# Performance work log

Hardware: AMD Instinct MI355X
Metric: run time of the kernel (lower is better)

Reference implementation:

```python
import jax, jax.numpy as jnp
import numpy as np
import math

IN_DIM = 256
HID_DIM = 256
NUM_EDGE_TYPES = 3
HEADS = 8
HEAD_DIM = HID_DIM // HEADS  # 32
QK_DIM = (NUM_EDGE_TYPES + 1) * HID_DIM  # 1024
N = 4096


def _glorot(key, shape):
    # torch_geometric-style glorot: uniform(-a, a), a = sqrt(6/(fan_in+fan_out)) over last two dims
    a = math.sqrt(6.0 / (shape[-2] + shape[-1]))
    return jax.random.uniform(key, shape, jnp.float32, -a, a)


def setup_inputs() -> dict:
    key = jax.random.key(0)
    ks = jax.random.split(key, 8)
    return {
        "input_x": jax.random.normal(ks[0], (N, IN_DIM), jnp.float32),
        "pe_Q": jax.random.normal(ks[1], (N, NUM_EDGE_TYPES * HID_DIM), jnp.float32),
        "pe_K": jax.random.normal(ks[2], (N, NUM_EDGE_TYPES * HID_DIM), jnp.float32),
        "A": jnp.zeros((N, N), jnp.int32),  # accepted by forward but unused
        "WQ": _glorot(ks[3], (HEADS, QK_DIM, HEAD_DIM)),
        "WK": _glorot(ks[4], (HEADS, QK_DIM, HEAD_DIM)),
        "WV": _glorot(ks[5], (HEADS, IN_DIM, HEAD_DIM)),
        "Q_bias": jnp.zeros((HEADS, 1, HEAD_DIM), jnp.float32),
        "K_bias": jnp.zeros((HEADS, 1, HEAD_DIM), jnp.float32),
        "V_bias": jnp.zeros((HEADS, 1, HEAD_DIM), jnp.float32),
        "lin_w": _glorot(ks[6], (HID_DIM, HID_DIM)),
        "lin_b": jnp.zeros((HID_DIM,), jnp.float32),
    }


def reference(input_x, pe_Q, pe_K, A, WQ, WK, WV, Q_bias, K_bias, V_bias, lin_w, lin_b):
    x_Q = jnp.concatenate([input_x, pe_Q], axis=-1)  # [N, QK_DIM]
    x_K = jnp.concatenate([input_x, pe_K], axis=-1)  # [N, QK_DIM]
    Q = jnp.einsum('nd,hdk->hnk', x_Q, WQ) + Q_bias   # [H, N, hd]
    K = jnp.einsum('nd,hdk->hnk', x_K, WK) + K_bias   # [H, N, hd]
    V = jnp.einsum('nd,hdk->hnk', input_x, WV) + V_bias
    scores = jnp.einsum('hnk,hmk->hnm', Q, K) / math.sqrt(HID_DIM)  # [H, N, N]
    scores = scores - jax.lax.stop_gradient(jnp.max(scores, axis=-1, keepdims=True))
    attn = jax.nn.softmax(scores, axis=-1)
    attn = jnp.where(jnp.isnan(attn), jnp.zeros_like(attn), attn)
    attn_x = jnp.einsum('hnm,hmk->hnk', attn, V)      # [H, N, hd]
    # cat(list over heads, dim=1) -> [N, H*hd] with head-major column order
    x_cat = jnp.transpose(attn_x, (1, 0, 2)).reshape(attn_x.shape[1], -1)
    return x_cat @ lin_w.T + lin_b
```

## Files before the change

### kernel.cpp

```cpp
#include <hip/hip_runtime.h>
#include <hip/hip_bf16.h>

typedef __attribute__((ext_vector_type(8))) short bf16x8;
typedef __attribute__((ext_vector_type(4))) float f32x4;

__device__ __forceinline__ unsigned short f2b(float f) {
    union { float f; unsigned int u; } v; v.f = f;
    unsigned int u = v.u;
    unsigned int r = (u + 0x7FFFu + ((u >> 16) & 1u)) >> 16;
    return (unsigned short)r;
}
__device__ __forceinline__ float b2f(unsigned short h) {
    union { unsigned int u; float f; } v; v.u = ((unsigned int)h) << 16;
    return v.f;
}
__device__ __forceinline__ unsigned pk2(float a, float b) {
    union { __hip_bfloat162 h; unsigned u; } c;
    c.h = __float22bfloat162_rn(make_float2(a, b));
    return c.u;
}

__global__ __launch_bounds__(256) void prep_main(
    const float* __restrict__ WQ, const float* __restrict__ WK,
    const float* __restrict__ WV, const float* __restrict__ LW,
    const float* __restrict__ Qb, const float* __restrict__ Kb,
    const float* __restrict__ Vb,
    const float* __restrict__ x, const float* __restrict__ peQ,
    const float* __restrict__ peK,
    unsigned short* __restrict__ WQt, unsigned short* __restrict__ WKt,
    unsigned short* __restrict__ WVt, unsigned short* __restrict__ LWt,
    unsigned short* __restrict__ Bq, unsigned short* __restrict__ Bk,
    unsigned short* __restrict__ Bv,
    unsigned short* __restrict__ xb, unsigned short* __restrict__ peQb,
    unsigned short* __restrict__ peKb) {
    int b = blockIdx.x, t = threadIdx.x;
    if (b < 288) {
        const float* W; unsigned short* Wt; int h, d0, D; float sc = 1.0f;
        if (b < 128)      { W = WQ; Wt = WQt; h = b >> 4;   d0 = (b & 15) * 64; D = 1024; sc = 0.0625f; }
        else if (b < 256) { int bb = b - 128; W = WK; Wt = WKt; h = bb >> 4; d0 = (bb & 15) * 64; D = 1024; }
        else              { int bb = b - 256; W = WV; Wt = WVt; h = bb >> 2; d0 = (bb & 3) * 64;  D = 256; }
        __shared__ float Ts[32][65];
        int dr = t >> 2, k0 = (t & 3) * 8;
        const float* src = W + (h * D + d0 + dr) * 32 + k0;
        float4 u0 = *(const float4*)src;
        float4 u1 = *(const float4*)(src + 4);
        Ts[k0 + 0][dr] = u0.x; Ts[k0 + 1][dr] = u0.y; Ts[k0 + 2][dr] = u0.z; Ts[k0 + 3][dr] = u0.w;
        Ts[k0 + 4][dr] = u1.x; Ts[k0 + 5][dr] = u1.y; Ts[k0 + 6][dr] = u1.z; Ts[k0 + 7][dr] = u1.w;
        __syncthreads();
        int k = t >> 3, dc = (t & 7) * 8;
        union { unsigned short s[8]; uint4 v; } pk;
#pragma unroll
        for (int i = 0; i < 8; i++) pk.s[i] = f2b(Ts[k][dc + i] * sc);
        *(uint4*)(Wt + (h * 32 + k) * D + d0 + dc) = pk.v;
    } else if (b < 320) {
        int base = (b - 288) * 2048 + t * 8;
        const float* sp = LW + base;
        float4 u0 = *(const float4*)sp;
        float4 u1 = *(const float4*)(sp + 4);
        union { unsigned u[4]; uint4 v; } pk;
        pk.u[0] = pk2(u0.x, u0.y); pk.u[1] = pk2(u0.z, u0.w);
        pk.u[2] = pk2(u1.x, u1.y); pk.u[3] = pk2(u1.z, u1.w);
        *(uint4*)(LWt + base) = pk.v;
    } else if (b == 320) {
        Bq[t] = f2b(Qb[t] * 0.0625f); Bk[t] = f2b(Kb[t]); Bv[t] = f2b(Vb[t]);
    } else {
        int idx = (b - 321) * 2048 + t * 8;
        const float* sp; unsigned short* dp;
        if (idx < 1048576)      { sp = x + idx;                dp = xb + idx; }
        else if (idx < 4194304) { sp = peQ + (idx - 1048576);  dp = peQb + (idx - 1048576); }
        else                    { sp = peK + (idx - 4194304);  dp = peKb + (idx - 4194304); }
        float4 u0 = *(const float4*)sp;
        float4 u1 = *(const float4*)(sp + 4);
        union { unsigned u[4]; uint4 v; } pk;
        pk.u[0] = pk2(u0.x, u0.y); pk.u[1] = pk2(u0.z, u0.w);
        pk.u[2] = pk2(u1.x, u1.y); pk.u[3] = pk2(u1.z, u1.w);
        *(uint4*)dp = pk.v;
    }
}

__global__ __launch_bounds__(256) void prep_fb(
    const float* __restrict__ WQ, const float* __restrict__ WK,
    const float* __restrict__ WV,
    const float* __restrict__ Qb, const float* __restrict__ Kb,
    const float* __restrict__ Vb,
    unsigned short* __restrict__ WQt, unsigned short* __restrict__ WKt,
    unsigned short* __restrict__ WVt,
    unsigned short* __restrict__ Bq, unsigned short* __restrict__ Bk,
    unsigned short* __restrict__ Bv) {
    int b = blockIdx.x, t = threadIdx.x;
    if (b < 288) {
        const float* W; unsigned short* Wt; int h, d0, D; float sc = 1.0f;
        if (b < 128)      { W = WQ; Wt = WQt; h = b >> 4;   d0 = (b & 15) * 64; D = 1024; sc = 0.0625f; }
        else if (b < 256) { int bb = b - 128; W = WK; Wt = WKt; h = bb >> 4; d0 = (bb & 15) * 64; D = 1024; }
        else              { int bb = b - 256; W = WV; Wt = WVt; h = bb >> 2; d0 = (bb & 3) * 64;  D = 256; }
        __shared__ float Ts[32][65];
        int dr = t >> 2, k0 = (t & 3) * 8;
        const float* src = W + (h * D + d0 + dr) * 32 + k0;
        float4 u0 = *(const float4*)src;
        float4 u1 = *(const float4*)(src + 4);
        Ts[k0 + 0][dr] = u0.x; Ts[k0 + 1][dr] = u0.y; Ts[k0 + 2][dr] = u0.z; Ts[k0 + 3][dr] = u0.w;
        Ts[k0 + 4][dr] = u1.x; Ts[k0 + 5][dr] = u1.y; Ts[k0 + 6][dr] = u1.z; Ts[k0 + 7][dr] = u1.w;
        __syncthreads();
        int k = t >> 3, dc = (t & 7) * 8;
        union { unsigned short s[8]; uint4 v; } pk;
#pragma unroll
        for (int i = 0; i < 8; i++) pk.s[i] = f2b(Ts[k][dc + i] * sc);
        *(uint4*)(Wt + (h * 32 + k) * D + d0 + dc) = pk.v;
    } else {
        Bq[t] = f2b(Qb[t] * 0.0625f); Bk[t] = f2b(Kb[t]); Bv[t] = f2b(Vb[t]);
    }
}

template <bool ABF16>
__global__ __launch_bounds__(256) void proj_fused(
    const void* __restrict__ xv,
    const void* __restrict__ peQv, const void* __restrict__ peKv,
    const unsigned short* __restrict__ WQt, const unsigned short* __restrict__ WKt,
    const unsigned short* __restrict__ WVt,
    const unsigned short* __restrict__ Bq, const unsigned short* __restrict__ Bk,
    const unsigned short* __restrict__ Bv,
    unsigned short* __restrict__ Qc, unsigned short* __restrict__ KV) {
    __shared__ unsigned short As[64 * 72];
    __shared__ unsigned short Bs[64 * 72];
    int bx = blockIdx.x;
    int which = bx >> 8, bb = bx & 255;
    const void* A1; const unsigned short* Bt; const unsigned short* bias; int K;
    if (which == 0)      { A1 = peQv; Bt = WQt; bias = Bq; K = 1024; }
    else if (which == 1) { A1 = peKv; Bt = WKt; bias = Bk; K = 1024; }
    else                 { A1 = peQv; Bt = WVt; bias = Bv; K = 256; }
    int mb = bb & 63, nb = bb >> 6;
    int m0 = mb * 64, n0 = nb * 64;
    int t = threadIdx.x, w = t >> 6, lane = t & 63;
    int ln = lane & 15, q8 = (lane >> 4) * 8;
    int wm = (w >> 1) * 32, wn = (w & 1) * 32;
    int sr = t >> 3, sc = (t & 7) * 8;
    f32x4 acc[2][2];
#pragma unroll
    for (int i = 0; i < 2; i++)
#pragma unroll
        for (int j = 0; j < 2; j++) acc[i][j] = (f32x4){0.f, 0.f, 0.f, 0.f};
    for (int kb = 0; kb < K; kb += 64) {
#pragma unroll
        for (int half = 0; half < 2; half++) {
            int r = sr + half * 32;
            int c = kb + sc;
            if (ABF16) {
                const unsigned short* ap = (c < 256)
                    ? ((const unsigned short*)xv + (m0 + r) * 256 + c)
                    : ((const unsigned short*)A1 + (m0 + r) * 768 + (c - 256));
                *(uint4*)&As[r * 72 + sc] = *(const uint4*)ap;
            } else {
                const float* ap = (c < 256)
                    ? ((const float*)xv + (m0 + r) * 256 + c)
                    : ((const float*)A1 + (m0 + r) * 768 + (c - 256));
                float4 u0 = *(const float4*)ap;
                float4 u1 = *(const float4*)(ap + 4);
                union { unsigned u[4]; uint4 v; } pk;
                pk.u[0] = pk2(u0.x, u0.y); pk.u[1] = pk2(u0.z, u0.w);
                pk.u[2] = pk2(u1.x, u1.y); pk.u[3] = pk2(u1.z, u1.w);
                *(uint4*)&As[r * 72 + sc] = pk.v;
            }
            *(uint4*)&Bs[r * 72 + sc] = *(const uint4*)(Bt + (n0 + r) * K + c);
        }
        __syncthreads();
#pragma unroll
        for (int ks = 0; ks < 64; ks += 32) {
            bf16x8 a[2], b[2];
#pragma unroll
            for (int i = 0; i < 2; i++) {
                a[i] = *(const bf16x8*)&As[(wm + i * 16 + ln) * 72 + ks + q8];
                b[i] = *(const bf16x8*)&Bs[(wn + i * 16 + ln) * 72 + ks + q8];
            }
#pragma unroll
            for (int i = 0; i < 2; i++)
#pragma unroll
                for (int j = 0; j < 2; j++)
                    acc[i][j] = __builtin_amdgcn_mfma_f32_16x16x32_bf16(a[i], b[j], acc[i][j], 0, 0, 0);
        }
        __syncthreads();
    }
#pragma unroll
    for (int j = 0; j < 2; j++) {
        int ncol = n0 + wn + j * 16 + ln;
        float bv = b2f(bias[ncol]);
        int h2 = ncol >> 5, din = ncol & 31;
#pragma unroll
        for (int i = 0; i < 2; i++) {
            int rbase = m0 + wm + i * 16 + ((lane >> 4) * 4);
            if (which == 0) {
#pragma unroll
                for (int r = 0; r < 4; r++)
                    Qc[(rbase + r) * 256 + ncol] = f2b(acc[i][j][r] + bv);
            } else if (which == 1) {
#pragma unroll
                for (int r = 0; r < 4; r++) {
                    int key = rbase + r;
                    int T2 = key >> 6, k6 = key & 63;
                    int kt = ((k6 >> 2) & 1) + ((k6 >> 4) & 2);
                    int ln2 = ((k6 >> 3) & 3) * 4 + (k6 & 3);
                    int addr = (h2 * 64 + T2) * 4096 + kt * 512
                             + ((din >> 3) * 16 + ln2) * 8 + (din & 7);
                    KV[addr] = f2b(acc[i][j][r] + bv);
                }
            } else {
                int key = rbase;
                int T2 = key >> 6, k6 = key & 63;
                int chunk = 4 + ((din >> 4) << 1) + ((k6 >> 5) & 1);
                int lane2 = ((k6 >> 3) & 3) * 16 + (din & 15);
                int addr = (h2 * 64 + T2) * 4096 + chunk * 512 + lane2 * 8 + (k6 & 7);
                uint2 vv;
                vv.x = pk2(acc[i][j][0] + bv, acc[i][j][1] + bv);
                vv.y = pk2(acc[i][j][2] + bv, acc[i][j][3] + bv);
                *(uint2*)(KV + addr) = vv;
            }
        }
    }
}

__global__ __launch_bounds__(256, 4) void attn_kernel(
    const unsigned short* __restrict__ Qc,
    const unsigned short* __restrict__ KV,
    unsigned short* __restrict__ Xc) {
    __shared__ float Om[4][32][33];
    __shared__ float Ls[4][32];
    int head = blockIdx.x >> 7;
    int qb = blockIdx.x & 127;
    int t = threadIdx.x, w = t >> 6, lane = t & 63;
    int ln = lane & 15, quad = lane >> 4, q8 = quad * 8;
    int q0 = qb * 32;
    bf16x8 qfv[2];
#pragma unroll
    for (int qf = 0; qf < 2; qf++)
        qfv[qf] = *(const bf16x8*)(Qc + (q0 + qf * 16 + ln) * 256 + head * 32 + q8);
    const unsigned short* kv = KV + (head * 64 + w * 16) * 4096 + lane * 8;
    f32x4 o[2][2];
#pragma unroll
    for (int qf = 0; qf < 2; qf++)
#pragma unroll
        for (int hh = 0; hh < 2; hh++) o[qf][hh] = (f32x4){0.f, 0.f, 0.f, 0.f};
    const f32x4 z = {0.f, 0.f, 0.f, 0.f};
    f32x4 lacc[2]; lacc[0] = z; lacc[1] = z;
    bf16x8 k0 = *(const bf16x8*)(kv + 0);
    bf16x8 k1 = *(const bf16x8*)(kv + 512);
    bf16x8 k2 = *(const bf16x8*)(kv + 1024);
    bf16x8 k3 = *(const bf16x8*)(kv + 1536);
    bf16x8 v0 = *(const bf16x8*)(kv + 2048);
    bf16x8 v1 = *(const bf16x8*)(kv + 2560);
    bf16x8 v2 = *(const bf16x8*)(kv + 3072);
    bf16x8 v3 = *(const bf16x8*)(kv + 3584);
#pragma unroll 1
    for (int it = 0; it < 16; it++) {
        int nit = (it < 15) ? (it + 1) : 15;
        const unsigned short* nkv = kv + nit * 4096;
        bf16x8 nk0 = *(const bf16x8*)(nkv + 0);
        bf16x8 nk1 = *(const bf16x8*)(nkv + 512);
        bf16x8 nk2 = *(const bf16x8*)(nkv + 1024);
        bf16x8 nk3 = *(const bf16x8*)(nkv + 1536);
        bf16x8 nv0 = *(const bf16x8*)(nkv + 2048);
        bf16x8 nv1 = *(const bf16x8*)(nkv + 2560);
        bf16x8 nv2 = *(const bf16x8*)(nkv + 3072);
        bf16x8 nv3 = *(const bf16x8*)(nkv + 3584);
#pragma unroll
        for (int qf = 0; qf < 2; qf++) {
            f32x4 s0 = __builtin_amdgcn_mfma_f32_16x16x32_bf16(k0, qfv[qf], z, 0, 0, 0);
            f32x4 s1 = __builtin_amdgcn_mfma_f32_16x16x32_bf16(k1, qfv[qf], z, 0, 0, 0);
            f32x4 s2 = __builtin_amdgcn_mfma_f32_16x16x32_bf16(k2, qfv[qf], z, 0, 0, 0);
            f32x4 s3 = __builtin_amdgcn_mfma_f32_16x16x32_bf16(k3, qfv[qf], z, 0, 0, 0);
            float p0[4], p1[4], p2[4], p3[4];
#pragma unroll
            for (int r = 0; r < 4; r++) {
                p0[r] = __expf(s0[r]); p1[r] = __expf(s1[r]);
                p2[r] = __expf(s2[r]); p3[r] = __expf(s3[r]);
            }
            f32x4 ps;
#pragma unroll
            for (int r = 0; r < 4; r++) ps[r] = (p0[r] + p1[r]) + (p2[r] + p3[r]);
            lacc[qf] += ps;
            union { unsigned u[4]; bf16x8 v; } b0, b1;
            b0.u[0] = pk2(p0[0], p0[1]); b0.u[1] = pk2(p0[2], p0[3]);
            b0.u[2] = pk2(p1[0], p1[1]); b0.u[3] = pk2(p1[2], p1[3]);
            b1.u[0] = pk2(p2[0], p2[1]); b1.u[1] = pk2(p2[2], p2[3]);
            b1.u[2] = pk2(p3[0], p3[1]); b1.u[3] = pk2(p3[2], p3[3]);
            o[qf][0] = __builtin_amdgcn_mfma_f32_16x16x32_bf16(v0, b0.v, o[qf][0], 0, 0, 0);
            o[qf][0] = __builtin_amdgcn_mfma_f32_16x16x32_bf16(v1, b1.v, o[qf][0], 0, 0, 0);
            o[qf][1] = __builtin_amdgcn_mfma_f32_16x16x32_bf16(v2, b0.v, o[qf][1], 0, 0, 0);
            o[qf][1] = __builtin_amdgcn_mfma_f32_16x16x32_bf16(v3, b1.v, o[qf][1], 0, 0, 0);
        }
        k0 = nk0; k1 = nk1; k2 = nk2; k3 = nk3;
        v0 = nv0; v1 = nv1; v2 = nv2; v3 = nv3;
    }
#pragma unroll
    for (int qf = 0; qf < 2; qf++) {
        float lts = (lacc[qf][0] + lacc[qf][1]) + (lacc[qf][2] + lacc[qf][3]);
        lts += __shfl_xor(lts, 16, 64);
        lts += __shfl_xor(lts, 32, 64);
#pragma unroll
        for (int r = 0; r < 4; r++) {
            Om[w][quad * 4 + r][qf * 16 + ln] = o[qf][0][r];
            Om[w][16 + quad * 4 + r][qf * 16 + ln] = o[qf][1][r];
        }
        if (quad == 0) Ls[w][qf * 16 + ln] = lts;
    }
    __syncthreads();
    int q = t & 31, d = (t >> 5) * 4;
    float num[4] = {0.f, 0.f, 0.f, 0.f};
    float den = 0.f;
#pragma unroll
    for (int w2 = 0; w2 < 4; w2++) {
        den += Ls[w2][q];
#pragma unroll
        for (int i = 0; i < 4; i++) num[i] += Om[w2][d + i][q];
    }
    float inv = 1.f / den;
    uint2 outv;
    outv.x = pk2(num[0] * inv, num[1] * inv);
    outv.y = pk2(num[2] * inv, num[3] * inv);
    *(uint2*)(Xc + (q0 + q) * 256 + head * 32 + d) = outv;
}

template <bool BBF16>
__global__ __launch_bounds__(256) void gemm_out(
    const unsigned short* __restrict__ A,
    const void* __restrict__ LWv,
    const float* __restrict__ Lb,
    float* __restrict__ C) {
    __shared__ unsigned short As[64 * 72];
    __shared__ unsigned short Bs[64 * 72];
    int mb = blockIdx.x & 63, nb = blockIdx.x >> 6;
    int m0 = mb * 64, n0 = nb * 64;
    int t = threadIdx.x, w = t >> 6, lane = t & 63;
    int ln = lane & 15, q8 = (lane >> 4) * 8;
    int wm = (w >> 1) * 32, wn = (w & 1) * 32;
    int sr = t >> 3, sc = (t & 7) * 8;
    f32x4 acc[2][2];
#pragma unroll
    for (int i = 0; i < 2; i++)
#pragma unroll
        for (int j = 0; j < 2; j++) acc[i][j] = (f32x4){0.f, 0.f, 0.f, 0.f};
    for (int kb = 0; kb < 256; kb += 64) {
#pragma unroll
        for (int half = 0; half < 2; half++) {
            int r = sr + half * 32;
            int c = kb + sc;
            *(uint4*)&As[r * 72 + sc] = *(const uint4*)(A + (m0 + r) * 256 + c);
            if (BBF16) {
                *(uint4*)&Bs[r * 72 + sc] =
                    *(const uint4*)((const unsigned short*)LWv + (n0 + r) * 256 + c);
            } else {
                const float* bp = (const float*)LWv + (n0 + r) * 256 + c;
                float4 u0 = *(const float4*)bp;
                float4 u1 = *(const float4*)(bp + 4);
                union { unsigned u[4]; uint4 v; } pk;
                pk.u[0] = pk2(u0.x, u0.y); pk.u[1] = pk2(u0.z, u0.w);
                pk.u[2] = pk2(u1.x, u1.y); pk.u[3] = pk2(u1.z, u1.w);
                *(uint4*)&Bs[r * 72 + sc] = pk.v;
            }
        }
        __syncthreads();
#pragma unroll
        for (int ks = 0; ks < 64; ks += 32) {
            bf16x8 a[2], b[2];
#pragma unroll
            for (int i = 0; i < 2; i++) {
                a[i] = *(const bf16x8*)&As[(wm + i * 16 + ln) * 72 + ks + q8];
                b[i] = *(const bf16x8*)&Bs[(wn + i * 16 + ln) * 72 + ks + q8];
            }
#pragma unroll
            for (int i = 0; i < 2; i++)
#pragma unroll
                for (int j = 0; j < 2; j++)
                    acc[i][j] = __builtin_amdgcn_mfma_f32_16x16x32_bf16(a[i], b[j], acc[i][j], 0, 0, 0);
        }
        __syncthreads();
    }
#pragma unroll
    for (int j = 0; j < 2; j++) {
        int ncol = n0 + wn + j * 16 + ln;
        float bv = Lb[ncol];
#pragma unroll
        for (int i = 0; i < 2; i++) {
            int rbase = m0 + wm + i * 16 + ((lane >> 4) * 4);
#pragma unroll
            for (int r = 0; r < 4; r++)
                C[(rbase + r) * 256 + ncol] = acc[i][j][r] + bv;
        }
    }
}

extern "C" void kernel_launch(void* const* d_in, const int* in_sizes, int n_in,
                              void* d_out, int out_size, void* d_ws, size_t ws_size,
                              hipStream_t stream) {
    const float* input_x = (const float*)d_in[0];
    const float* pe_Q    = (const float*)d_in[1];
    const float* pe_K    = (const float*)d_in[2];
    const float* WQ = (const float*)d_in[4];
    const float* WK = (const float*)d_in[5];
    const float* WV = (const float*)d_in[6];
    const float* Qb = (const float*)d_in[7];
    const float* Kb = (const float*)d_in[8];
    const float* Vb = (const float*)d_in[9];
    const float* lw = (const float*)d_in[10];
    const float* lb = (const float*)d_in[11];
    float* outp = (float*)d_out;

    unsigned short* ws = (unsigned short*)d_ws;
    unsigned short* WQt = ws;
    unsigned short* WKt = WQt + 262144;
    unsigned short* WVt = WKt + 262144;
    unsigned short* LWt = WVt + 65536;
    unsigned short* Bq  = LWt + 65536;
    unsigned short* Bk  = Bq + 256;
    unsigned short* Bv  = Bk + 256;
    unsigned short* xb   = Bv + 256;
    unsigned short* peQb = xb + 1048576;
    unsigned short* peKb = peQb + 3145728;
    unsigned short* Qc   = peKb + 3145728;
    unsigned short* KVb  = Qc + 1048576;
    unsigned short* Xc   = KVb + 2097152;
    size_t need = (size_t)(Xc + 1048576 - ws) * 2;

    if (ws_size >= need) {
        prep_main<<<dim3(3905), dim3(256), 0, stream>>>(
            WQ, WK, WV, lw, Qb, Kb, Vb, input_x, pe_Q, pe_K,
            WQt, WKt, WVt, LWt, Bq, Bk, Bv, xb, peQb, peKb);
        proj_fused<true><<<dim3(768), dim3(256), 0, stream>>>(
            xb, peQb, peKb, WQt, WKt, WVt, Bq, Bk, Bv, Qc, KVb);
        attn_kernel<<<dim3(1024), dim3(256), 0, stream>>>(Qc, KVb, Xc);
        gemm_out<true><<<dim3(256), dim3(256), 0, stream>>>(Xc, LWt, lb, outp);
    } else {
        unsigned short* Qc2  = Bv + 256;
        unsigned short* KV2  = Qc2 + 1048576;
        unsigned short* Xc2  = KV2 + 2097152;
        prep_fb<<<dim3(289), dim3(256), 0, stream>>>(WQ, WK, WV, Qb, Kb, Vb,
                                                     WQt, WKt, WVt, Bq, Bk, Bv);
        proj_fused<false><<<dim3(768), dim3(256), 0, stream>>>(
            input_x, pe_Q, pe_K, WQt, WKt, WVt, Bq, Bk, Bv, Qc2, KV2);
        attn_kernel<<<dim3(1024), dim3(256), 0, stream>>>(Qc2, KV2, Xc2);
        gemm_out<false><<<dim3(256), dim3(256), 0, stream>>>(Xc2, lw, lb, outp);
    }
}
```

Before: 179.6 us.

## Enlarge attention query tile to 64 with 8 waves and fold log2e into Q scale

The attention kernel now gives each 512-thread block 64 queries instead of 32, spread across 8 waves that each handle 8 key tiles. Blocks are ordered head-fastest, and the explicit register prefetch of the next K/V tile is dropped. The softmax exponent uses the hardware exp2 with log2(e) folded into the Q weight and bias scale, which saves a multiply per score. The larger tile reuses each K/V load across more queries, at the cost of a bigger LDS reduction buffer, more registers per wave and no manual load/compute overlap.

```diff
diff --git a/kernel.cpp b/kernel.cpp
--- a/kernel.cpp
+++ b/kernel.cpp
@@ -3,6 +3,8 @@
 
 typedef __attribute__((ext_vector_type(8))) short bf16x8;
 typedef __attribute__((ext_vector_type(4))) float f32x4;
+
+#define QSCALE 0.09016844f
 
 __device__ __forceinline__ unsigned short f2b(float f) {
     union { float f; unsigned int u; } v; v.f = f;
@@ -36,7 +38,7 @@
     int b = blockIdx.x, t = threadIdx.x;
     if (b < 288) {
         const float* W; unsigned short* Wt; int h, d0, D; float sc = 1.0f;
-        if (b < 128)      { W = WQ; Wt = WQt; h = b >> 4;   d0 = (b & 15) * 64; D = 1024; sc = 0.0625f; }
+        if (b < 128)      { W = WQ; Wt = WQt; h = b >> 4;   d0 = (b & 15) * 64; D = 1024; sc = QSCALE; }
         else if (b < 256) { int bb = b - 128; W = WK; Wt = WKt; h = bb >> 4; d0 = (bb & 15) * 64; D = 1024; }
         else              { int bb = b - 256; W = WV; Wt = WVt; h = bb >> 2; d0 = (bb & 3) * 64;  D = 256; }
         __shared__ float Ts[32][65];
@@ -62,7 +64,7 @@
         pk.u[2] = pk2(u1.x, u1.y); pk.u[3] = pk2(u1.z, u1.w);
         *(uint4*)(LWt + base) = pk.v;
     } else if (b == 320) {
-        Bq[t] = f2b(Qb[t] * 0.0625f); Bk[t] = f2b(Kb[t]); Bv[t] = f2b(Vb[t]);
+        Bq[t] = f2b(Qb[t] * QSCALE); Bk[t] = f2b(Kb[t]); Bv[t] = f2b(Vb[t]);
     } else {
         int idx = (b - 321) * 2048 + t * 8;
         const float* sp; unsigned short* dp;
@@ -90,7 +92,7 @@
     int b = blockIdx.x, t = threadIdx.x;
     if (b < 288) {
         const float* W; unsigned short* Wt; int h, d0, D; float sc = 1.0f;
-        if (b < 128)      { W = WQ; Wt = WQt; h = b >> 4;   d0 = (b & 15) * 64; D = 1024; sc = 0.0625f; }
+        if (b < 128)      { W = WQ; Wt = WQt; h = b >> 4;   d0 = (b & 15) * 64; D = 1024; sc = QSCALE; }
         else if (b < 256) { int bb = b - 128; W = WK; Wt = WKt; h = bb >> 4; d0 = (bb & 15) * 64; D = 1024; }
         else              { int bb = b - 256; W = WV; Wt = WVt; h = bb >> 2; d0 = (bb & 3) * 64;  D = 256; }
         __shared__ float Ts[32][65];
@@ -107,7 +109,7 @@
         for (int i = 0; i < 8; i++) pk.s[i] = f2b(Ts[k][dc + i] * sc);
         *(uint4*)(Wt + (h * 32 + k) * D + d0 + dc) = pk.v;
     } else {
-        Bq[t] = f2b(Qb[t] * 0.0625f); Bk[t] = f2b(Kb[t]); Bv[t] = f2b(Vb[t]);
+        Bq[t] = f2b(Qb[t] * QSCALE); Bk[t] = f2b(Kb[t]); Bv[t] = f2b(Vb[t]);
     }
 }
 
@@ -217,51 +219,42 @@
     }
 }
 
-__global__ __launch_bounds__(256, 4) void attn_kernel(
+__global__ __launch_bounds__(512, 4) void attn_kernel(
     const unsigned short* __restrict__ Qc,
     const unsigned short* __restrict__ KV,
     unsigned short* __restrict__ Xc) {
-    __shared__ float Om[4][32][33];
-    __shared__ float Ls[4][32];
-    int head = blockIdx.x >> 7;
-    int qb = blockIdx.x & 127;
+    __shared__ float Om[8][32][65];
+    __shared__ float Ls[8][64];
+    int head = blockIdx.x & 7;
+    int qb = blockIdx.x >> 3;
     int t = threadIdx.x, w = t >> 6, lane = t & 63;
     int ln = lane & 15, quad = lane >> 4, q8 = quad * 8;
-    int q0 = qb * 32;
-    bf16x8 qfv[2];
-#pragma unroll
-    for (int qf = 0; qf < 2; qf++)
+    int q0 = qb * 64;
+    bf16x8 qfv[4];
+#pragma unroll
+    for (int qf = 0; qf < 4; qf++)
         qfv[qf] = *(const bf16x8*)(Qc + (q0 + qf * 16 + ln) * 256 + head * 32 + q8);
-    const unsigned short* kv = KV + (head * 64 + w * 16) * 4096 + lane * 8;
-    f32x4 o[2][2];
-#pragma unroll
-    for (int qf = 0; qf < 2; qf++)
+    const unsigned short* kv = KV + (head * 64 + w * 8) * 4096 + lane * 8;
+    f32x4 o[4][2];
+    float lts[4] = {0.f, 0.f, 0.f, 0.f};
+#pragma unroll
+    for (int qf = 0; qf < 4; qf++)
 #pragma unroll
         for (int hh = 0; hh < 2; hh++) o[qf][hh] = (f32x4){0.f, 0.f, 0.f, 0.f};
     const f32x4 z = {0.f, 0.f, 0.f, 0.f};
-    f32x4 lacc[2]; lacc[0] = z; lacc[1] = z;
-    bf16x8 k0 = *(const bf16x8*)(kv + 0);
-    bf16x8 k1 = *(const bf16x8*)(kv + 512);
-    bf16x8 k2 = *(const bf16x8*)(kv + 1024);
-    bf16x8 k3 = *(const bf16x8*)(kv + 1536);
-    bf16x8 v0 = *(const bf16x8*)(kv + 2048);
-    bf16x8 v1 = *(const bf16x8*)(kv + 2560);
-    bf16x8 v2 = *(const bf16x8*)(kv + 3072);
-    bf16x8 v3 = *(const bf16x8*)(kv + 3584);
 #pragma unroll 1
-    for (int it = 0; it < 16; it++) {
-        int nit = (it < 15) ? (it + 1) : 15;
-        const unsigned short* nkv = kv + nit * 4096;
-        bf16x8 nk0 = *(const bf16x8*)(nkv + 0);
-        bf16x8 nk1 = *(const bf16x8*)(nkv + 512);
-        bf16x8 nk2 = *(const bf16x8*)(nkv + 1024);
-        bf16x8 nk3 = *(const bf16x8*)(nkv + 1536);
-        bf16x8 nv0 = *(const bf16x8*)(nkv + 2048);
-        bf16x8 nv1 = *(const bf16x8*)(nkv + 2560);
-        bf16x8 nv2 = *(const bf16x8*)(nkv + 3072);
-        bf16x8 nv3 = *(const bf16x8*)(nkv + 3584);
-#pragma unroll
-        for (int qf = 0; qf < 2; qf++) {
+    for (int it = 0; it < 8; it++) {
+        const unsigned short* ckv = kv + it * 4096;
+        bf16x8 k0 = *(const bf16x8*)(ckv + 0);
+        bf16x8 k1 = *(const bf16x8*)(ckv + 512);
+        bf16x8 k2 = *(const bf16x8*)(ckv + 1024);
+        bf16x8 k3 = *(const bf16x8*)(ckv + 1536);
+        bf16x8 v0 = *(const bf16x8*)(ckv + 2048);
+        bf16x8 v1 = *(const bf16x8*)(ckv + 2560);
+        bf16x8 v2 = *(const bf16x8*)(ckv + 3072);
+        bf16x8 v3 = *(const bf16x8*)(ckv + 3584);
+#pragma unroll
+        for (int qf = 0; qf < 4; qf++) {
             f32x4 s0 = __builtin_amdgcn_mfma_f32_16x16x32_bf16(k0, qfv[qf], z, 0, 0, 0);
             f32x4 s1 = __builtin_amdgcn_mfma_f32_16x16x32_bf16(k1, qfv[qf], z, 0, 0, 0);
             f32x4 s2 = __builtin_amdgcn_mfma_f32_16x16x32_bf16(k2, qfv[qf], z, 0, 0, 0);
@@ -269,13 +262,15 @@
             float p0[4], p1[4], p2[4], p3[4];
 #pragma unroll
             for (int r = 0; r < 4; r++) {
-                p0[r] = __expf(s0[r]); p1[r] = __expf(s1[r]);
-                p2[r] = __expf(s2[r]); p3[r] = __expf(s3[r]);
-            }
-            f32x4 ps;
-#pragma unroll
-            for (int r = 0; r < 4; r++) ps[r] = (p0[r] + p1[r]) + (p2[r] + p3[r]);
-            lacc[qf] += ps;
+                p0[r] = __builtin_amdgcn_exp2f(s0[r]);
+                p1[r] = __builtin_amdgcn_exp2f(s1[r]);
+                p2[r] = __builtin_amdgcn_exp2f(s2[r]);
+                p3[r] = __builtin_amdgcn_exp2f(s3[r]);
+            }
+            float psum = 0.f;
+#pragma unroll
+            for (int r = 0; r < 4; r++) psum += (p0[r] + p1[r]) + (p2[r] + p3[r]);
+            lts[qf] += psum;
             union { unsigned u[4]; bf16x8 v; } b0, b1;
             b0.u[0] = pk2(p0[0], p0[1]); b0.u[1] = pk2(p0[2], p0[3]);
             b0.u[2] = pk2(p1[0], p1[1]); b0.u[3] = pk2(p1[2], p1[3]);
@@ -286,27 +281,25 @@
             o[qf][1] = __builtin_amdgcn_mfma_f32_16x16x32_bf16(v2, b0.v, o[qf][1], 0, 0, 0);
             o[qf][1] = __builtin_amdgcn_mfma_f32_16x16x32_bf16(v3, b1.v, o[qf][1], 0, 0, 0);
         }
-        k0 = nk0; k1 = nk1; k2 = nk2; k3 = nk3;
-        v0 = nv0; v1 = nv1; v2 = nv2; v3 = nv3;
-    }
-#pragma unroll
-    for (int qf = 0; qf < 2; qf++) {
-        float lts = (lacc[qf][0] + lacc[qf][1]) + (lacc[qf][2] + lacc[qf][3]);
-        lts += __shfl_xor(lts, 16, 64);
-        lts += __shfl_xor(lts, 32, 64);
+    }
+#pragma unroll
+    for (int qf = 0; qf < 4; qf++) {
+        float l = lts[qf];
+        l += __shfl_xor(l, 16, 64);
+        l += __shfl_xor(l, 32, 64);
 #pragma unroll
         for (int r = 0; r < 4; r++) {
             Om[w][quad * 4 + r][qf * 16 + ln] = o[qf][0][r];
             Om[w][16 + quad * 4 + r][qf * 16 + ln] = o[qf][1][r];
         }
-        if (quad == 0) Ls[w][qf * 16 + ln] = lts;
+        if (quad == 0) Ls[w][qf * 16 + ln] = l;
     }
     __syncthreads();
-    int q = t & 31, d = (t >> 5) * 4;
+    int q = t & 63, d = (t >> 6) * 4;
     float num[4] = {0.f, 0.f, 0.f, 0.f};
     float den = 0.f;
 #pragma unroll
-    for (int w2 = 0; w2 < 4; w2++) {
+    for (int w2 = 0; w2 < 8; w2++) {
         den += Ls[w2][q];
 #pragma unroll
         for (int i = 0; i < 4; i++) num[i] += Om[w2][d + i][q];
@@ -425,7 +418,7 @@
             WQt, WKt, WVt, LWt, Bq, Bk, Bv, xb, peQb, peKb);
         proj_fused<true><<<dim3(768), dim3(256), 0, stream>>>(
             xb, peQb, peKb, WQt, WKt, WVt, Bq, Bk, Bv, Qc, KVb);
-        attn_kernel<<<dim3(1024), dim3(256), 0, stream>>>(Qc, KVb, Xc);
+        attn_kernel<<<dim3(512), dim3(512), 0, stream>>>(Qc, KVb, Xc);
         gemm_out<true><<<dim3(256), dim3(256), 0, stream>>>(Xc, LWt, lb, outp);
     } else {
         unsigned short* Qc2  = Bv + 256;
@@ -435,7 +428,7 @@
                                                      WQt, WKt, WVt, Bq, Bk, Bv);
         proj_fused<false><<<dim3(768), dim3(256), 0, stream>>>(
             input_x, pe_Q, pe_K, WQt, WKt, WVt, Bq, Bk, Bv, Qc2, KV2);
-        attn_kernel<<<dim3(1024), dim3(256), 0, stream>>>(Qc2, KV2, Xc2);
+        attn_kernel<<<dim3(512), dim3(512), 0, stream>>>(Qc2, KV2, Xc2);
         gemm_out<false><<<dim3(256), dim3(256), 0, stream>>>(Xc2, lw, lb, outp);
     }
 }
```

New measurement: 182.3 us. Within noise of the previous version (+1.5%).

## Use exp2 with folded log2e scale and 64-query attention blocks of 512 threads

Applied to the files above, without the earlier changes.

Folds log2(e) into the Q scale so the softmax can use the hardware exp2 instruction instead of __expf. Attention blocks now hold 8 waves covering 64 queries, with 4 key-splitting waves per 32-query group, and the block index is reordered to head-minor. The point is to share K/V tile loads across more queries per block and cut per-element exp cost. The row-sum accumulation moves to a scalar per query fragment. The larger block may lower occupancy and use more shared memory for the partial-output reduction.

```diff
diff --git a/kernel.cpp b/kernel.cpp
--- a/kernel.cpp
+++ b/kernel.cpp
@@ -3,6 +3,8 @@
 
 typedef __attribute__((ext_vector_type(8))) short bf16x8;
 typedef __attribute__((ext_vector_type(4))) float f32x4;
+
+#define QSCALE 0.09016844f
 
 __device__ __forceinline__ unsigned short f2b(float f) {
     union { float f; unsigned int u; } v; v.f = f;
@@ -36,7 +38,7 @@
     int b = blockIdx.x, t = threadIdx.x;
     if (b < 288) {
         const float* W; unsigned short* Wt; int h, d0, D; float sc = 1.0f;
-        if (b < 128)      { W = WQ; Wt = WQt; h = b >> 4;   d0 = (b & 15) * 64; D = 1024; sc = 0.0625f; }
+        if (b < 128)      { W = WQ; Wt = WQt; h = b >> 4;   d0 = (b & 15) * 64; D = 1024; sc = QSCALE; }
         else if (b < 256) { int bb = b - 128; W = WK; Wt = WKt; h = bb >> 4; d0 = (bb & 15) * 64; D = 1024; }
         else              { int bb = b - 256; W = WV; Wt = WVt; h = bb >> 2; d0 = (bb & 3) * 64;  D = 256; }
         __shared__ float Ts[32][65];
@@ -62,7 +64,7 @@
         pk.u[2] = pk2(u1.x, u1.y); pk.u[3] = pk2(u1.z, u1.w);
         *(uint4*)(LWt + base) = pk.v;
     } else if (b == 320) {
-        Bq[t] = f2b(Qb[t] * 0.0625f); Bk[t] = f2b(Kb[t]); Bv[t] = f2b(Vb[t]);
+        Bq[t] = f2b(Qb[t] * QSCALE); Bk[t] = f2b(Kb[t]); Bv[t] = f2b(Vb[t]);
     } else {
         int idx = (b - 321) * 2048 + t * 8;
         const float* sp; unsigned short* dp;
@@ -90,7 +92,7 @@
     int b = blockIdx.x, t = threadIdx.x;
     if (b < 288) {
         const float* W; unsigned short* Wt; int h, d0, D; float sc = 1.0f;
-        if (b < 128)      { W = WQ; Wt = WQt; h = b >> 4;   d0 = (b & 15) * 64; D = 1024; sc = 0.0625f; }
+        if (b < 128)      { W = WQ; Wt = WQt; h = b >> 4;   d0 = (b & 15) * 64; D = 1024; sc = QSCALE; }
         else if (b < 256) { int bb = b - 128; W = WK; Wt = WKt; h = bb >> 4; d0 = (bb & 15) * 64; D = 1024; }
         else              { int bb = b - 256; W = WV; Wt = WVt; h = bb >> 2; d0 = (bb & 3) * 64;  D = 256; }
         __shared__ float Ts[32][65];
@@ -107,7 +109,7 @@
         for (int i = 0; i < 8; i++) pk.s[i] = f2b(Ts[k][dc + i] * sc);
         *(uint4*)(Wt + (h * 32 + k) * D + d0 + dc) = pk.v;
     } else {
-        Bq[t] = f2b(Qb[t] * 0.0625f); Bk[t] = f2b(Kb[t]); Bv[t] = f2b(Vb[t]);
+        Bq[t] = f2b(Qb[t] * QSCALE); Bk[t] = f2b(Kb[t]); Bv[t] = f2b(Vb[t]);
     }
 }
 
@@ -217,29 +219,30 @@
     }
 }
 
-__global__ __launch_bounds__(256, 4) void attn_kernel(
+__global__ __launch_bounds__(512, 4) void attn_kernel(
     const unsigned short* __restrict__ Qc,
     const unsigned short* __restrict__ KV,
     unsigned short* __restrict__ Xc) {
-    __shared__ float Om[4][32][33];
-    __shared__ float Ls[4][32];
-    int head = blockIdx.x >> 7;
-    int qb = blockIdx.x & 127;
+    __shared__ float Om[8][32][33];
+    __shared__ float Ls[8][32];
+    int head = blockIdx.x & 7;
+    int qb = blockIdx.x >> 3;
     int t = threadIdx.x, w = t >> 6, lane = t & 63;
     int ln = lane & 15, quad = lane >> 4, q8 = quad * 8;
-    int q0 = qb * 32;
+    int wq = w >> 2, wk = w & 3;
+    int q0 = qb * 64;
     bf16x8 qfv[2];
 #pragma unroll
     for (int qf = 0; qf < 2; qf++)
-        qfv[qf] = *(const bf16x8*)(Qc + (q0 + qf * 16 + ln) * 256 + head * 32 + q8);
-    const unsigned short* kv = KV + (head * 64 + w * 16) * 4096 + lane * 8;
+        qfv[qf] = *(const bf16x8*)(Qc + (q0 + wq * 32 + qf * 16 + ln) * 256 + head * 32 + q8);
+    const unsigned short* kv = KV + (head * 64 + wk * 16) * 4096 + lane * 8;
     f32x4 o[2][2];
+    float lts[2] = {0.f, 0.f};
 #pragma unroll
     for (int qf = 0; qf < 2; qf++)
 #pragma unroll
         for (int hh = 0; hh < 2; hh++) o[qf][hh] = (f32x4){0.f, 0.f, 0.f, 0.f};
     const f32x4 z = {0.f, 0.f, 0.f, 0.f};
-    f32x4 lacc[2]; lacc[0] = z; lacc[1] = z;
     bf16x8 k0 = *(const bf16x8*)(kv + 0);
     bf16x8 k1 = *(const bf16x8*)(kv + 512);
     bf16x8 k2 = *(const bf16x8*)(kv + 1024);
@@ -269,13 +272,15 @@
             float p0[4], p1[4], p2[4], p3[4];
 #pragma unroll
             for (int r = 0; r < 4; r++) {
-                p0[r] = __expf(s0[r]); p1[r] = __expf(s1[r]);
-                p2[r] = __expf(s2[r]); p3[r] = __expf(s3[r]);
-            }
-            f32x4 ps;
-#pragma unroll
-            for (int r = 0; r < 4; r++) ps[r] = (p0[r] + p1[r]) + (p2[r] + p3[r]);
-            lacc[qf] += ps;
+                p0[r] = __builtin_amdgcn_exp2f(s0[r]);
+                p1[r] = __builtin_amdgcn_exp2f(s1[r]);
+                p2[r] = __builtin_amdgcn_exp2f(s2[r]);
+                p3[r] = __builtin_amdgcn_exp2f(s3[r]);
+            }
+            float psum = 0.f;
+#pragma unroll
+            for (int r = 0; r < 4; r++) psum += (p0[r] + p1[r]) + (p2[r] + p3[r]);
+            lts[qf] += psum;
             union { unsigned u[4]; bf16x8 v; } b0, b1;
             b0.u[0] = pk2(p0[0], p0[1]); b0.u[1] = pk2(p0[2], p0[3]);
             b0.u[2] = pk2(p1[0], p1[1]); b0.u[3] = pk2(p1[2], p1[3]);
@@ -291,31 +296,33 @@
     }
 #pragma unroll
     for (int qf = 0; qf < 2; qf++) {
-        float lts = (lacc[qf][0] + lacc[qf][1]) + (lacc[qf][2] + lacc[qf][3]);
-        lts += __shfl_xor(lts, 16, 64);
-        lts += __shfl_xor(lts, 32, 64);
+        float l = lts[qf];
+        l += __shfl_xor(l, 16, 64);
+        l += __shfl_xor(l, 32, 64);
 #pragma unroll
         for (int r = 0; r < 4; r++) {
             Om[w][quad * 4 + r][qf * 16 + ln] = o[qf][0][r];
             Om[w][16 + quad * 4 + r][qf * 16 + ln] = o[qf][1][r];
         }
-        if (quad == 0) Ls[w][qf * 16 + ln] = lts;
+        if (quad == 0) Ls[w][qf * 16 + ln] = l;
     }
     __syncthreads();
-    int q = t & 31, d = (t >> 5) * 4;
+    int q6 = t & 63, d = (t >> 6) * 4;
+    int g = q6 >> 5, ql = q6 & 31;
     float num[4] = {0.f, 0.f, 0.f, 0.f};
     float den = 0.f;
 #pragma unroll
     for (int w2 = 0; w2 < 4; w2++) {
-        den += Ls[w2][q];
-#pragma unroll
-        for (int i = 0; i < 4; i++) num[i] += Om[w2][d + i][q];
+        int ws2 = g * 4 + w2;
+        den += Ls[ws2][ql];
+#pragma unroll
+        for (int i = 0; i < 4; i++) num[i] += Om[ws2][d + i][ql];
     }
     float inv = 1.f / den;
     uint2 outv;
     outv.x = pk2(num[0] * inv, num[1] * inv);
     outv.y = pk2(num[2] * inv, num[3] * inv);
-    *(uint2*)(Xc + (q0 + q) * 256 + head * 32 + d) = outv;
+    *(uint2*)(Xc + (q0 + q6) * 256 + head * 32 + d) = outv;
 }
 
 template <bool BBF16>
@@ -425,7 +432,7 @@
             WQt, WKt, WVt, LWt, Bq, Bk, Bv, xb, peQb, peKb);
         proj_fused<true><<<dim3(768), dim3(256), 0, stream>>>(
             xb, peQb, peKb, WQt, WKt, WVt, Bq, Bk, Bv, Qc, KVb);
-        attn_kernel<<<dim3(1024), dim3(256), 0, stream>>>(Qc, KVb, Xc);
+        attn_kernel<<<dim3(512), dim3(512), 0, stream>>>(Qc, KVb, Xc);
         gemm_out<true><<<dim3(256), dim3(256), 0, stream>>>(Xc, LWt, lb, outp);
     } else {
         unsigned short* Qc2  = Bv + 256;
@@ -435,7 +442,7 @@
                                                      WQt, WKt, WVt, Bq, Bk, Bv);
         proj_fused<false><<<dim3(768), dim3(256), 0, stream>>>(
             input_x, pe_Q, pe_K, WQt, WKt, WVt, Bq, Bk, Bv, Qc2, KV2);
-        attn_kernel<<<dim3(1024), dim3(256), 0, stream>>>(Qc2, KV2, Xc2);
+        attn_kernel<<<dim3(512), dim3(512), 0, stream>>>(Qc2, KV2, Xc2);
         gemm_out<false><<<dim3(256), dim3(256), 0, stream>>>(Xc2, lw, lb, outp);
     }
 }
```

After: 177.1 us. No clear change (-1.4%).
